# Optimization experiments

Hardware: AMD Instinct MI355X
Metric: run time of the kernel (lower is better)

## Reference

```python
import jax, jax.numpy as jnp
import numpy as np

T, B, CIN, CRES, H, W = 48, 32, 2, 64, 34, 34
OUT, NPART, K = 10, 3, 3
ALPHA, BETA, THR = 0.9, 0.9, 1.0


def conv2d(x, w, b, pad):
    # x: [B,C,H,W], w: [O,I,K,K] (NCHW/OIHW), stride 1
    y = jax.lax.conv_general_dilated(
        x, w, window_strides=(1, 1), padding=[(pad, pad), (pad, pad)],
        dimension_numbers=('NCHW', 'OIHW', 'NCHW'))
    return y + b[None, :, None, None]


def setup_inputs() -> dict:
    key = jax.random.key(0)
    ks = jax.random.split(key, 9)
    x = jax.random.normal(ks[0], (T, B, CIN, H, W), dtype=jnp.float32)
    w_in = jax.random.normal(ks[1], (CRES, CIN, K, K), dtype=jnp.float32) * 0.2
    b_in = jax.random.normal(ks[2], (CRES,), dtype=jnp.float32) * 0.05
    w_rec = jax.random.normal(ks[3], (CRES, CRES, K, K), dtype=jnp.float32) * 0.04
    b_rec = jax.random.normal(ks[4], (CRES,), dtype=jnp.float32) * 0.05
    w_r1 = jax.random.normal(ks[5], (OUT, CRES * NPART, K, K), dtype=jnp.float32) * 0.02
    b_r1 = jax.random.normal(ks[6], (OUT,), dtype=jnp.float32) * 0.05
    w_r2 = jax.random.normal(ks[7], (OUT, OUT * H * W), dtype=jnp.float32) * 0.01
    b_r2 = jax.random.normal(ks[8], (OUT,), dtype=jnp.float32) * 0.05
    return {"x": x, "w_in": w_in, "b_in": b_in, "w_rec": w_rec, "b_rec": b_rec,
            "w_r1": w_r1, "b_r1": b_r1, "w_r2": w_r2, "b_r2": b_r2}


def reference(x, w_in, b_in, w_rec, b_rec, w_r1, b_r1, w_r2, b_r2):
    dt = x.dtype

    def step(carry, x_t):
        spk, syn, mem = carry
        cur = conv2d(x_t, w_in, b_in, pad=1)                      # input conv
        reset = (mem > THR).astype(dt)                            # snntorch mem_reset(prev mem)
        syn_n = ALPHA * syn + cur + conv2d(spk, w_rec, b_rec, 1)  # synaptic decay + recurrence
        mem_n = BETA * mem + syn_n - reset * THR                  # membrane update, subtract reset
        spk_n = (mem_n > THR).astype(dt)                          # fire
        return (spk_n, syn_n, mem_n), spk_n

    z = jnp.zeros((B, CRES, H, W), dt)
    _, spk_rec = jax.lax.scan(step, (z, z, z), x)                 # [T,B,CRES,H,W]

    ps = T // NPART
    parts = spk_rec[:NPART * ps].reshape(NPART, ps, B, CRES, H, W).mean(axis=1)
    ro_in = jnp.transpose(parts, (1, 0, 2, 3, 4)).reshape(B, NPART * CRES, H, W)
    y = conv2d(ro_in, w_r1, b_r1, pad=1)                          # [B,OUT,34,34]
    y = y.reshape(B, -1) @ w_r2.T + b_r2                          # [B,OUT]
    out = jax.nn.softmax(y, axis=1)
    return out, spk_rec
```

## Files before the change

kernel.cpp:

```cpp
#include <hip/hip_runtime.h>
#include <math.h>

#define TT   48
#define BB   32
#define CINC 2
#define CR   64
#define HH   34
#define WW   34
#define HWW  (HH*WW)
#define PWP  36
#define PHWP (36*36)
#define NOUT 10
#define NP   3
#define OG   8
#define RCH  6

__global__ __launch_bounds__(256) void transpose_weights(
    const float* __restrict__ w_in,
    const float* __restrict__ w_rec,
    float* __restrict__ wiT,
    float* __restrict__ wrT)
{
    const int i = blockIdx.x*256 + threadIdx.x;
    if (i < 576*64) {
        const int k = i >> 6, o = i & 63;
        const int tap = k >> 6, ci = k & 63;
        wrT[i] = w_rec[o*576 + ci*9 + tap];
    }
    if (i < 18*64) {
        const int k = i >> 6, o = i & 63;
        const int tap = k >> 1, ci = k & 1;
        wiT[i] = w_in[o*18 + ci*9 + tap];
    }
}

__global__ __launch_bounds__(256) void step_kernel(
    const float* __restrict__ x,
    const float* __restrict__ wiT,
    const float* __restrict__ b_in,
    const float* __restrict__ wrT,
    const float* __restrict__ b_rec,
    const unsigned char* __restrict__ sp_rd,
    unsigned char*       __restrict__ sp_wr,
    float* __restrict__ syn,
    float* __restrict__ mem,
    float* __restrict__ spk_rec,
    unsigned char* __restrict__ partsum,
    int t)
{
    #pragma clang fp contract(off)

    const int p = blockIdx.y*256 + threadIdx.x;
    if (p >= HWW) return;
    const int b  = blockIdx.x;
    const int og = blockIdx.z * OG;
    const int part = t >> 4;
    const int h = p / WW;
    const int w = p - h*WW;

    const float* xb = x + (size_t)((t*BB + b)*CINC)*HWW;
    const unsigned char* spb = sp_rd + (size_t)b*CR*PHWP;

    float cin[OG];
    #pragma unroll
    for (int j = 0; j < OG; ++j) cin[j] = 0.0f;
    #pragma unroll
    for (int kh = 0; kh < 3; ++kh) {
        const int ih = h + kh - 1;
        if ((unsigned)ih >= (unsigned)HH) continue;
        #pragma unroll
        for (int kw = 0; kw < 3; ++kw) {
            const int iw = w + kw - 1;
            if ((unsigned)iw >= (unsigned)WW) continue;
            #pragma unroll
            for (int ci = 0; ci < CINC; ++ci) {
                const float s = xb[ci*HWW + ih*WW + iw];
                const float* wr = wiT + ((kh*3+kw)*2 + ci)*64 + og;
                #pragma unroll
                for (int j = 0; j < OG; ++j)
                    cin[j] = fmaf(wr[j], s, cin[j]);
            }
        }
    }

    float acc[OG];
    #pragma unroll
    for (int j = 0; j < OG; ++j) acc[j] = 0.0f;
    const unsigned char* sp0 = spb + h*PWP + w;
    #pragma unroll 1
    for (int tap = 0; tap < 9; ++tap) {
        const int kh = tap / 3;
        const int kw = tap - kh*3;
        const unsigned char* sp_t = sp0 + kh*PWP + kw;
        const float* wbase = wrT + (size_t)tap*64*64 + og;
        #pragma unroll 8
        for (int ci = 0; ci < CR; ++ci) {
            const float s = (float)sp_t[(size_t)ci*PHWP];
            const float* wr = wbase + ci*64;
            #pragma unroll
            for (int j = 0; j < OG; ++j)
                acc[j] = fmaf(wr[j], s, acc[j]);
        }
    }

    #pragma unroll
    for (int j = 0; j < OG; ++j) {
        const int o = og + j;
        const size_t so = ((size_t)b*CR + o)*HWW + p;
        const float cur = cin[j] + b_in[o];
        const float rec = acc[j] + b_rec[o];
        const float syn_v = syn[so];
        const float m     = mem[so];
        const float sv = fmaf(0.9f, syn_v, cur) + rec;
        const float reset = (m > 1.0f) ? 1.0f : 0.0f;
        const float mn = fmaf(0.9f, m, sv) - reset;
        const int fire = (mn > 1.0f) ? 1 : 0;

        syn[so] = sv;
        mem[so] = mn;
        spk_rec[((size_t)(t*BB + b)*CR + o)*HWW + p] = (float)fire;
        sp_wr[((size_t)b*CR + o)*PHWP + (h+1)*PWP + (w+1)] =
            (unsigned char)fire;
        unsigned char* ps = partsum + ((size_t)(part*BB + b)*CR + o)*HWW + p;
        *ps = (unsigned char)(*ps + fire);
    }
}

__global__ __launch_bounds__(256) void readout_conv_part(
    const unsigned char* __restrict__ partsum,
    const float* __restrict__ w_r1,
    double* __restrict__ y1p)
{
    const int b = blockIdx.x;
    const int p = blockIdx.y * 256 + threadIdx.x;
    if (p >= HWW) return;
    const int z = blockIdx.z;
    const int h = p / WW;
    const int w = p - h*WW;

    double acc[NOUT];
    #pragma unroll
    for (int j = 0; j < NOUT; ++j) acc[j] = 0.0;

    const int pc0 = z * (NP*CR/RCH);
    for (int pc = pc0; pc < pc0 + NP*CR/RCH; ++pc) {
        const int part = pc >> 6;
        const int c    = pc & 63;
        const unsigned char* src =
            partsum + ((size_t)(part*BB + b)*CR + c)*HWW;

        double v[9];
        #pragma unroll
        for (int kh = 0; kh < 3; ++kh) {
            const int ih = h + kh - 1;
            #pragma unroll
            for (int kw = 0; kw < 3; ++kw) {
                const int iw = w + kw - 1;
                const bool ok = ((unsigned)ih < (unsigned)HH) &&
                                ((unsigned)iw < (unsigned)WW);
                v[kh*3+kw] = ok ? (double)src[ih*WW + iw] * 0.0625 : 0.0;
            }
        }
        #pragma unroll
        for (int j = 0; j < NOUT; ++j) {
            const float* wj = w_r1 + ((size_t)j*NP*CR + pc)*9;
            #pragma unroll
            for (int k = 0; k < 9; ++k)
                acc[j] = fma((double)wj[k], v[k], acc[j]);
        }
    }
    #pragma unroll
    for (int j = 0; j < NOUT; ++j)
        y1p[(((size_t)z*BB + b)*NOUT + j)*HWW + p] = acc[j];
}

__global__ __launch_bounds__(256) void readout_conv_reduce(
    const double* __restrict__ y1p,
    const float* __restrict__ b_r1,
    double* __restrict__ y1)
{
    const int b = blockIdx.x;
    const int p = blockIdx.y * 256 + threadIdx.x;
    if (p >= HWW) return;
    #pragma unroll
    for (int j = 0; j < NOUT; ++j) {
        double s = (double)b_r1[j];
        #pragma unroll
        for (int z = 0; z < RCH; ++z)
            s += y1p[(((size_t)z*BB + b)*NOUT + j)*HWW + p];
        y1[((size_t)b*NOUT + j)*HWW + p] = s;
    }
}

__global__ __launch_bounds__(256) void readout_fc(
    const double* __restrict__ y1,
    const float* __restrict__ w_r2,
    const float* __restrict__ b_r2,
    float* __restrict__ out)
{
    const int b = blockIdx.x;
    const double* yb = y1 + (size_t)b*NOUT*HWW;

    double acc[NOUT];
    #pragma unroll
    for (int o = 0; o < NOUT; ++o) acc[o] = 0.0;

    for (int i = threadIdx.x; i < NOUT*HWW; i += 256) {
        const double v = yb[i];
        #pragma unroll
        for (int o = 0; o < NOUT; ++o)
            acc[o] = fma(v, (double)w_r2[(size_t)o*NOUT*HWW + i], acc[o]);
    }

    const int lane = threadIdx.x & 63;
    const int wv   = threadIdx.x >> 6;
    __shared__ double wsum[4][NOUT];

    #pragma unroll
    for (int o = 0; o < NOUT; ++o) {
        double v = acc[o];
        #pragma unroll
        for (int off = 32; off > 0; off >>= 1) v += __shfl_down(v, off);
        if (lane == 0) wsum[wv][o] = v;
    }
    __syncthreads();

    if (threadIdx.x == 0) {
        double s[NOUT];
        double mx = -1e300;
        #pragma unroll
        for (int o = 0; o < NOUT; ++o) {
            s[o] = wsum[0][o] + wsum[1][o] + wsum[2][o] + wsum[3][o]
                 + (double)b_r2[o];
            mx = fmax(mx, s[o]);
        }
        double den = 0.0;
        #pragma unroll
        for (int o = 0; o < NOUT; ++o) { s[o] = exp(s[o] - mx); den += s[o]; }
        #pragma unroll
        for (int o = 0; o < NOUT; ++o) out[b*NOUT + o] = (float)(s[o] / den);
    }
}

extern "C" void kernel_launch(void* const* d_in, const int* in_sizes, int n_in,
                              void* d_out, int out_size, void* d_ws, size_t ws_size,
                              hipStream_t stream)
{
    const float* x     = (const float*)d_in[0];
    const float* w_in  = (const float*)d_in[1];
    const float* b_in  = (const float*)d_in[2];
    const float* w_rec = (const float*)d_in[3];
    const float* b_rec = (const float*)d_in[4];
    const float* w_r1  = (const float*)d_in[5];
    const float* b_r1  = (const float*)d_in[6];
    const float* w_r2  = (const float*)d_in[7];
    const float* b_r2  = (const float*)d_in[8];

    float* out     = (float*)d_out;
    float* spk_rec = out + BB*NOUT;

    const size_t n_state = (size_t)BB*CR*HWW;
    const size_t n_pad   = (size_t)BB*CR*PHWP;
    const size_t n_part  = (size_t)NP*BB*CR*HWW;
    const size_t n_y1    = (size_t)BB*NOUT*HWW;

    char* ws = (char*)d_ws;
    float*         syn     = (float*)ws;             ws += n_state*4;
    float*         mem     = (float*)ws;             ws += n_state*4;
    unsigned char* pad0    = (unsigned char*)ws;     ws += n_pad;
    unsigned char* pad1    = (unsigned char*)ws;     ws += n_pad;
    unsigned char* partsum = (unsigned char*)ws;     ws += n_part;
    double*        y1      = (double*)ws;            ws += n_y1*8;
    double*        y1p     = (double*)ws;            ws += (size_t)RCH*n_y1*8;
    float*         wiT     = (float*)ws;             ws += 18*64*4;
    float*         wrT     = (float*)ws;             ws += 576*64*4;

    const size_t zero_bytes = n_state*8 + 2*n_pad + n_part;
    hipMemsetAsync(d_ws, 0, zero_bytes, stream);

    transpose_weights<<<(576*64 + 255)/256, 256, 0, stream>>>(
        w_in, w_rec, wiT, wrT);

    for (int t = 0; t < TT; ++t) {
        const unsigned char* rd = (t & 1) ? pad1 : pad0;
        unsigned char*       wr = (t & 1) ? pad0 : pad1;
        step_kernel<<<dim3(BB, 5, CR/OG), 256, 0, stream>>>(
            x, wiT, b_in, wrT, b_rec,
            rd, wr, syn, mem, spk_rec, partsum, t);
    }

    readout_conv_part<<<dim3(BB, 5, RCH), 256, 0, stream>>>(partsum, w_r1, y1p);
    readout_conv_reduce<<<dim3(BB, 5), 256, 0, stream>>>(y1p, b_r1, y1);
    readout_fc<<<BB, 256, 0, stream>>>(y1, w_r2, b_r2, out);
}
```

Before: 2.732 ms.

## Store padded spike buffers channel-last and load 16 channels per vector read

The padded uint8 spike buffer moves from [B][C][36][36] to [B][36][36][64], so the 64 input channels of each tap are contiguous. The recurrent conv loop then reads them with four 16-byte uint4 loads and unpacks the bytes, replacing 64 strided byte loads per tap. Each block packs its 8 output channels' spikes into one 64-bit store. Neighbouring threads now read addresses 64 bytes apart, which changes coalescing, and the byte unpacking adds ALU work.

```diff
diff --git a/kernel.cpp b/kernel.cpp
--- a/kernel.cpp
+++ b/kernel.cpp
@@ -59,7 +59,7 @@
     const int w = p - h*WW;
 
     const float* xb = x + (size_t)((t*BB + b)*CINC)*HWW;
-    const unsigned char* spb = sp_rd + (size_t)b*CR*PHWP;
+    const unsigned char* spb = sp_rd + (size_t)b*PHWP*64;
 
     float cin[OG];
     #pragma unroll
@@ -86,23 +86,43 @@
     float acc[OG];
     #pragma unroll
     for (int j = 0; j < OG; ++j) acc[j] = 0.0f;
-    const unsigned char* sp0 = spb + h*PWP + w;
     #pragma unroll 1
     for (int tap = 0; tap < 9; ++tap) {
         const int kh = tap / 3;
         const int kw = tap - kh*3;
-        const unsigned char* sp_t = sp0 + kh*PWP + kw;
+        const uint4* qp = (const uint4*)(spb
+                          + (size_t)((h+kh)*PWP + (w+kw))*64);
         const float* wbase = wrT + (size_t)tap*64*64 + og;
-        #pragma unroll 8
-        for (int ci = 0; ci < CR; ++ci) {
-            const float s = (float)sp_t[(size_t)ci*PHWP];
-            const float* wr = wbase + ci*64;
+        #pragma unroll
+        for (int g = 0; g < 4; ++g) {
+            const uint4 v = qp[g];
+            const unsigned int dw0 = v.x, dw1 = v.y, dw2 = v.z, dw3 = v.w;
+            const unsigned int dws[4] = {dw0, dw1, dw2, dw3};
             #pragma unroll
-            for (int j = 0; j < OG; ++j)
-                acc[j] = fmaf(wr[j], s, acc[j]);
-        }
-    }
-
+            for (int dd = 0; dd < 4; ++dd) {
+                const unsigned int d = dws[dd];
+                const float s0 = (float)(d & 0xffu);
+                const float s1 = (float)((d >> 8) & 0xffu);
+                const float s2 = (float)((d >> 16) & 0xffu);
+                const float s3 = (float)(d >> 24);
+                const float* w0 = wbase + (g*16 + dd*4 + 0)*64;
+                #pragma unroll
+                for (int j = 0; j < OG; ++j)
+                    acc[j] = fmaf(w0[j],      s0, acc[j]);
+                #pragma unroll
+                for (int j = 0; j < OG; ++j)
+                    acc[j] = fmaf(w0[64+j],   s1, acc[j]);
+                #pragma unroll
+                for (int j = 0; j < OG; ++j)
+                    acc[j] = fmaf(w0[128+j],  s2, acc[j]);
+                #pragma unroll
+                for (int j = 0; j < OG; ++j)
+                    acc[j] = fmaf(w0[192+j],  s3, acc[j]);
+            }
+        }
+    }
+
+    unsigned long long pk = 0ull;
     #pragma unroll
     for (int j = 0; j < OG; ++j) {
         const int o = og + j;
@@ -119,11 +139,12 @@
         syn[so] = sv;
         mem[so] = mn;
         spk_rec[((size_t)(t*BB + b)*CR + o)*HWW + p] = (float)fire;
-        sp_wr[((size_t)b*CR + o)*PHWP + (h+1)*PWP + (w+1)] =
-            (unsigned char)fire;
+        pk |= (unsigned long long)fire << (8*j);
         unsigned char* ps = partsum + ((size_t)(part*BB + b)*CR + o)*HWW + p;
         *ps = (unsigned char)(*ps + fire);
     }
+    *(unsigned long long*)(sp_wr
+        + ((size_t)b*PHWP + (size_t)(h+1)*PWP + (w+1))*64 + og) = pk;
 }
 
 __global__ __launch_bounds__(256) void readout_conv_part(
@@ -260,7 +281,7 @@
     float* spk_rec = out + BB*NOUT;
 
     const size_t n_state = (size_t)BB*CR*HWW;
-    const size_t n_pad   = (size_t)BB*CR*PHWP;
+    const size_t n_pad   = (size_t)BB*PHWP*64;
     const size_t n_part  = (size_t)NP*BB*CR*HWW;
     const size_t n_y1    = (size_t)BB*NOUT*HWW;
 
```

Result: slower. 3.063 ms (+12.1%).
